# Performance work log

Measured on AMD Instinct MI355X. Metric: run time of the kernel, lower is better.

## Reference

```python
import jax, jax.numpy as jnp
import numpy as np

N_NODES = 100000
N_EDGES = 3200000
N_GRAPHS = 256
IN_CH = 8
HID = 64


def _gcn_conv(x, W, b, src, dst, n):
    # PyG GCNConv default: add self-loops, symmetric normalization.
    # out_i = sum_{j->i} d_i^-1/2 d_j^-1/2 (xW)_j + (1/d_i)(xW)_i + b
    xw = x @ W                                     # [N, out]
    deg = jax.ops.segment_sum(jnp.ones_like(dst, dtype=xw.dtype), dst,
                              num_segments=n) + 1.0  # +1 for self-loop
    dinv = jax.lax.rsqrt(deg)
    norm = dinv[src] * dinv[dst]                   # [E]
    agg = jax.ops.segment_sum(xw[src] * norm[:, None], dst, num_segments=n)
    agg = agg + xw * (1.0 / deg)[:, None]          # self-loop term (norm = 1/deg)
    return agg + b


def setup_inputs() -> dict:
    key = jax.random.key(0)
    ks = jax.random.split(key, 12)
    x = jax.random.normal(ks[0], (N_NODES, IN_CH), dtype=jnp.float32)
    edge_index = jax.random.randint(ks[1], (2, N_EDGES), 0, N_NODES, dtype=jnp.int64)
    batch = jnp.sort(jax.random.randint(ks[2], (N_NODES,), 0, N_GRAPHS, dtype=jnp.int64))

    def glorot(k, fan_in, fan_out):
        s = jnp.sqrt(2.0 / (fan_in + fan_out)).astype(jnp.float32)
        return jax.random.normal(k, (fan_in, fan_out), dtype=jnp.float32) * s

    return {
        "x": x, "edge_index": edge_index, "batch": batch,
        "W1": glorot(ks[3], IN_CH, HID), "b1": jnp.zeros((HID,), jnp.float32),
        "W2": glorot(ks[4], HID, 2 * HID), "b2": jnp.zeros((2 * HID,), jnp.float32),
        "W3": glorot(ks[5], 2 * HID, HID), "b3": jnp.zeros((HID,), jnp.float32),
        "Wl1": glorot(ks[6], HID, HID // 2), "bl1": jnp.zeros((HID // 2,), jnp.float32),
        "Wl2": glorot(ks[7], HID // 2, 1), "bl2": jnp.zeros((1,), jnp.float32),
    }


def reference(x, edge_index, batch, W1, b1, W2, b2, W3, b3, Wl1, bl1, Wl2, bl2):
    src, dst = edge_index[0], edge_index[1]
    h = jax.nn.relu(_gcn_conv(x, W1, b1, src, dst, N_NODES))
    h = jax.nn.relu(_gcn_conv(h, W2, b2, src, dst, N_NODES))
    h = jax.nn.relu(_gcn_conv(h, W3, b3, src, dst, N_NODES))
    # global mean pool over graphs
    sums = jax.ops.segment_sum(h, batch, num_segments=N_GRAPHS)
    cnts = jax.ops.segment_sum(jnp.ones((N_NODES,), h.dtype), batch, num_segments=N_GRAPHS)
    g = sums / jnp.maximum(cnts, 1.0)[:, None]     # [G, HID]
    g = jax.nn.relu(g @ Wl1 + bl1)
    out = g @ Wl2 + bl2                            # [G, 1]
    return out[:, 0]
```

## Files before the change

### kernel.cpp

```cpp
#include <hip/hip_runtime.h>
#include <hip/hip_bf16.h>

#define N_NODES 100000
#define N_EDGES 3200000
#define N_GRAPHS 256
#define NB_BUCKETS 196
#define BSHIFT 9
#define NBLK 256
#define SCAN_BLKS 49
#define CSR_CAP 22528

#define OFF_SUMS      0u
#define OFF_CNTF      65536u
#define ZERO_BYTES    66560u
#define OFF_HIST      66560u
#define OFF_BSUM      267264u
#define OFF_ROWPTR    267776u
#define OFF_DINV      668160u
#define OFF_COL       1068544u
#define OFF_XS1       13868544u
#define OFF_BUFQ      20268544u
#define OFF_BUFR      45868544u
#define OFF_BUFP      71468544u
#define OFF_PAIRS     OFF_BUFP

typedef __attribute__((ext_vector_type(8))) short bf16x8;
typedef __attribute__((ext_vector_type(4))) float f32x4;

__device__ __forceinline__ unsigned short f2bf(float f) {
    unsigned u = __float_as_uint(f);
    return (unsigned short)((u + 0x7fffu + ((u >> 16) & 1u)) >> 16);
}

__device__ __forceinline__ float bf2f(unsigned short h) {
    return __uint_as_float(((unsigned)h) << 16);
}

__device__ __forceinline__ void acc_bf8(uint4 v, float m, float* a) {
    a[0] += m * __uint_as_float(v.x << 16);
    a[1] += m * __uint_as_float(v.x & 0xffff0000u);
    a[2] += m * __uint_as_float(v.y << 16);
    a[3] += m * __uint_as_float(v.y & 0xffff0000u);
    a[4] += m * __uint_as_float(v.z << 16);
    a[5] += m * __uint_as_float(v.z & 0xffff0000u);
    a[6] += m * __uint_as_float(v.w << 16);
    a[7] += m * __uint_as_float(v.w & 0xffff0000u);
}

__global__ __launch_bounds__(256) void hist_kernel(const int* __restrict__ dst,
                                                   int* __restrict__ hist,
                                                   int* __restrict__ zbase,
                                                   int E, int epb) {
    __shared__ int h[NB_BUCKETS];
    int t = threadIdx.x, blk = blockIdx.x;
    int gid = blk * 256 + t;
    if (gid < (int)(ZERO_BYTES / 4)) zbase[gid] = 0;
    if (t < NB_BUCKETS) h[t] = 0;
    __syncthreads();
    int e0 = blk * epb, e1 = min(e0 + epb, E);
    for (int e = e0 + t; e < e1; e += 256)
        atomicAdd(&h[__builtin_nontemporal_load(&dst[e]) >> BSHIFT], 1);
    __syncthreads();
    if (t < NB_BUCKETS) hist[t * NBLK + blk] = h[t];
}

__global__ __launch_bounds__(1024) void scanhA_kernel(int* __restrict__ hist,
                                                      int* __restrict__ bsum) {
    __shared__ int s[1024];
    int t = threadIdx.x;
    int i = blockIdx.x * 1024 + t;
    int v = hist[i];
    s[t] = v;
    __syncthreads();
    for (int off = 1; off < 1024; off <<= 1) {
        int add = (t >= off) ? s[t - off] : 0;
        __syncthreads();
        s[t] += add;
        __syncthreads();
    }
    hist[i] = s[t] - v;
    if (t == 1023) bsum[blockIdx.x] = s[t];
}

__global__ __launch_bounds__(256) void bin_kernel(const int* __restrict__ src,
                                                  const int* __restrict__ dst,
                                                  const int* __restrict__ hist,
                                                  const int* __restrict__ bsum,
                                                  int* __restrict__ packed, int E, int epb) {
    __shared__ int cur[NB_BUCKETS];
    __shared__ int boffL[SCAN_BLKS];
    int t = threadIdx.x, blk = blockIdx.x;
    if (t < 64) {
        int orig = (t < SCAN_BLKS) ? bsum[t] : 0;
        int v = orig;
        for (int off = 1; off < 64; off <<= 1) {
            int up = __shfl_up(v, off);
            if (t >= off) v += up;
        }
        if (t < SCAN_BLKS) boffL[t] = v - orig;
    }
    __syncthreads();
    if (t < NB_BUCKETS) {
        int i = t * NBLK + blk;
        cur[t] = hist[i] + boffL[i >> 10];
    }
    __syncthreads();
    int e0 = blk * epb, e1 = min(e0 + epb, E);
    for (int e = e0 + t; e < e1; e += 256) {
        int d = __builtin_nontemporal_load(&dst[e]);
        int sv = __builtin_nontemporal_load(&src[e]);
        int pos = atomicAdd(&cur[d >> BSHIFT], 1);
        packed[pos] = ((d & 511) << 17) | sv;
    }
}

__global__ __launch_bounds__(512) void csr_kernel(const int* __restrict__ packed,
                                                  const int* __restrict__ hist,
                                                  const int* __restrict__ bsum,
                                                  const float* __restrict__ x,
                                                  int* __restrict__ row_ptr,
                                                  float* __restrict__ dinv,
                                                  unsigned short* __restrict__ xs1,
                                                  int* __restrict__ col, int E) {
    __shared__ int cntL[512];
    __shared__ int rsL[512];
    __shared__ int fillL[512];
    __shared__ int boffL[SCAN_BLKS];
    __shared__ int srcL[CSR_CAP];
    int t = threadIdx.x, b = blockIdx.x;
    int lo = b << BSHIFT;
    int nloc = min(512, N_NODES - lo);
    cntL[t] = 0;
    fillL[t] = 0;
    if (t < 64) {
        int orig = (t < SCAN_BLKS) ? bsum[t] : 0;
        int v = orig;
        for (int off = 1; off < 64; off <<= 1) {
            int up = __shfl_up(v, off);
            if (t >= off) v += up;
        }
        if (t < SCAN_BLKS) boffL[t] = v - orig;
    }
    __syncthreads();
    int i0 = b * NBLK;
    int start = hist[i0] + boffL[i0 >> 10];
    int end;
    if (b == NB_BUCKETS - 1) end = E;
    else {
        int i1 = (b + 1) * NBLK;
        end = hist[i1] + boffL[i1 >> 10];
    }
    for (int e = start + t; e < end; e += 512)
        atomicAdd(&cntL[packed[e] >> 17], 1);
    __syncthreads();
    int v = cntL[t];
    __syncthreads();
    for (int off = 1; off < 512; off <<= 1) {
        int add = (t >= off) ? cntL[t - off] : 0;
        __syncthreads();
        cntL[t] += add;
        __syncthreads();
    }
    int rowstart = start + cntL[t] - v;
    rsL[t] = rowstart;
    if (t < nloc) {
        int node = lo + t;
        row_ptr[node] = rowstart;
        float d = rsqrtf((float)(v + 1));
        dinv[node] = d;
        const float4* xv = reinterpret_cast<const float4*>(x) + node * 2;
        float4 xa = xv[0], xb = xv[1];
        uint4 p;
        p.x = (unsigned)f2bf(xa.x * d) | ((unsigned)f2bf(xa.y * d) << 16);
        p.y = (unsigned)f2bf(xa.z * d) | ((unsigned)f2bf(xa.w * d) << 16);
        p.z = (unsigned)f2bf(xb.x * d) | ((unsigned)f2bf(xb.y * d) << 16);
        p.w = (unsigned)f2bf(xb.z * d) | ((unsigned)f2bf(xb.w * d) << 16);
        *reinterpret_cast<uint4*>(&xs1[node * 8]) = p;
    }
    if (b == NB_BUCKETS - 1 && t == 0) row_ptr[N_NODES] = E;
    __syncthreads();
    for (int e = start + t; e < end; e += 512) {
        int p = packed[e];
        int dl = p >> 17;
        int pos = rsL[dl] + atomicAdd(&fillL[dl], 1);
        int rel = pos - start;
        if (rel < CSR_CAP) srcL[rel] = p & 0x1FFFF;
        else col[pos] = p & 0x1FFFF;
    }
    __syncthreads();
    int lim = min(end - start, CSR_CAP);
    for (int i = t; i < lim; i += 512)
        col[start + i] = srcL[i];
}

__global__ __launch_bounds__(256) void agg8g1_kernel(
        const unsigned short* __restrict__ xs, const int* __restrict__ row_ptr,
        const int* __restrict__ col, const float* __restrict__ dinv,
        const float* __restrict__ W1, const float* __restrict__ b1,
        unsigned short* __restrict__ xs2, int n) {
    int wave = threadIdx.x >> 6;
    int node = blockIdx.x * 4 + wave;
    if (node >= n) return;
    int lane = threadIdx.x & 63;
    int f = lane & 7;
    int s = lane >> 3;
    float w[8];
    float bias = b1[lane];
#pragma unroll
    for (int k = 0; k < 8; ++k) w[k] = W1[k * 64 + lane];
    int e0 = row_ptr[node], e1 = row_ptr[node + 1];
    float a = (s == 0) ? bf2f(xs[node * 8 + f]) : 0.0f;
    int base = e0;
    for (; e1 - base > 48; base += 48) {
#pragma unroll
        for (int g = 0; g < 6; ++g) {
            int c = __builtin_nontemporal_load(&col[base + 8 * g + s]);
            a += bf2f(xs[c * 8 + f]);
        }
    }
    int rem = e1 - base;
    if (rem > 0) {
        int e1m1 = e1 - 1;
        bool g4 = rem > 32, g5 = rem > 40;
        int i0 = base + s,      i1 = base + 8 + s,  i2 = base + 16 + s;
        int i3 = base + 24 + s, i4 = base + 32 + s, i5 = base + 40 + s;
        int c0 = __builtin_nontemporal_load(&col[min(i0, e1m1)]);
        int c1 = __builtin_nontemporal_load(&col[min(i1, e1m1)]);
        int c2 = __builtin_nontemporal_load(&col[min(i2, e1m1)]);
        int c3 = __builtin_nontemporal_load(&col[min(i3, e1m1)]);
        int c4 = 0, c5 = 0;
        if (g4) c4 = __builtin_nontemporal_load(&col[min(i4, e1m1)]);
        if (g5) c5 = __builtin_nontemporal_load(&col[min(i5, e1m1)]);
        float v0 = bf2f(xs[c0 * 8 + f]);
        float v1 = bf2f(xs[c1 * 8 + f]);
        float v2 = bf2f(xs[c2 * 8 + f]);
        float v3 = bf2f(xs[c3 * 8 + f]);
        float v4 = 0.f, v5 = 0.f;
        if (g4) v4 = bf2f(xs[c4 * 8 + f]);
        if (g5) v5 = bf2f(xs[c5 * 8 + f]);
        a += ((i0 < e1) ? v0 : 0.f) + ((i1 < e1) ? v1 : 0.f);
        a += ((i2 < e1) ? v2 : 0.f) + ((i3 < e1) ? v3 : 0.f);
        if (g4) a += (i4 < e1) ? v4 : 0.f;
        if (g5) a += (i5 < e1) ? v5 : 0.f;
    }
    a += __shfl_xor(a, 8);
    a += __shfl_xor(a, 16);
    a += __shfl_xor(a, 32);
    float d = dinv[node];
    float zd = a * d;
    float acc = bias;
#pragma unroll
    for (int k = 0; k < 8; ++k) acc += __shfl(zd, k) * w[k];
    xs2[node * 64 + lane] = f2bf(d * fmaxf(acc, 0.0f));
}

__global__ __launch_bounds__(256) void agg64bf_kernel(
        const unsigned short* __restrict__ xs, const int* __restrict__ row_ptr,
        const int* __restrict__ col, const float* __restrict__ dinv,
        unsigned short* __restrict__ z, int n0, int n1) {
    int wave = threadIdx.x >> 6;
    int node = n0 + blockIdx.x * 4 + wave;
    if (node >= n1) return;
    int lane = threadIdx.x & 63;
    int j = lane >> 3, l = lane & 7;
    int e0 = row_ptr[node], e1 = row_ptr[node + 1];
    float a[8] = {0.f, 0.f, 0.f, 0.f, 0.f, 0.f, 0.f, 0.f};
    uint4 sv = *reinterpret_cast<const uint4*>(&xs[node * 64 + 8 * l]);
    int base = e0;
    for (; e1 - base > 48; base += 32) {
        int s0 = __builtin_nontemporal_load(&col[base + j]);
        int s1 = __builtin_nontemporal_load(&col[base + 8 + j]);
        int s2 = __builtin_nontemporal_load(&col[base + 16 + j]);
        int s3 = __builtin_nontemporal_load(&col[base + 24 + j]);
        uint4 v0 = *reinterpret_cast<const uint4*>(&xs[s0 * 64 + 8 * l]);
        uint4 v1 = *reinterpret_cast<const uint4*>(&xs[s1 * 64 + 8 * l]);
        uint4 v2 = *reinterpret_cast<const uint4*>(&xs[s2 * 64 + 8 * l]);
        uint4 v3 = *reinterpret_cast<const uint4*>(&xs[s3 * 64 + 8 * l]);
        acc_bf8(v0, 1.f, a); acc_bf8(v1, 1.f, a);
        acc_bf8(v2, 1.f, a); acc_bf8(v3, 1.f, a);
    }
    int rem = e1 - base;
    if (rem > 0) {
        int e1m1 = e1 - 1;
        bool g4 = rem > 32, g5 = rem > 40;
        int i0 = base + j,      i1 = base + 8 + j;
        int i2 = base + 16 + j, i3 = base + 24 + j;
        int i4 = base + 32 + j, i5 = base + 40 + j;
        int c0 = __builtin_nontemporal_load(&col[min(i0, e1m1)]);
        int c1 = __builtin_nontemporal_load(&col[min(i1, e1m1)]);
        int c2 = __builtin_nontemporal_load(&col[min(i2, e1m1)]);
        int c3 = __builtin_nontemporal_load(&col[min(i3, e1m1)]);
        int c4 = 0, c5 = 0;
        if (g4) c4 = __builtin_nontemporal_load(&col[min(i4, e1m1)]);
        if (g5) c5 = __builtin_nontemporal_load(&col[min(i5, e1m1)]);
        uint4 v0 = *reinterpret_cast<const uint4*>(&xs[c0 * 64 + 8 * l]);
        uint4 v1 = *reinterpret_cast<const uint4*>(&xs[c1 * 64 + 8 * l]);
        uint4 v2 = *reinterpret_cast<const uint4*>(&xs[c2 * 64 + 8 * l]);
        uint4 v3 = *reinterpret_cast<const uint4*>(&xs[c3 * 64 + 8 * l]);
        uint4 v4, v5;
        if (g4) v4 = *reinterpret_cast<const uint4*>(&xs[c4 * 64 + 8 * l]);
        if (g5) v5 = *reinterpret_cast<const uint4*>(&xs[c5 * 64 + 8 * l]);
        acc_bf8(v0, (i0 < e1) ? 1.f : 0.f, a);
        acc_bf8(v1, (i1 < e1) ? 1.f : 0.f, a);
        acc_bf8(v2, (i2 < e1) ? 1.f : 0.f, a);
        acc_bf8(v3, (i3 < e1) ? 1.f : 0.f, a);
        if (g4) acc_bf8(v4, (i4 < e1) ? 1.f : 0.f, a);
        if (g5) acc_bf8(v5, (i5 < e1) ? 1.f : 0.f, a);
    }
    acc_bf8(sv, (j == 0) ? 1.f : 0.f, a);
#pragma unroll
    for (int k = 0; k < 8; ++k) {
        a[k] += __shfl_xor(a[k], 8);
        a[k] += __shfl_xor(a[k], 16);
        a[k] += __shfl_xor(a[k], 32);
    }
    if (j == 0) {
        float d = dinv[node];
        uint4 p;
        p.x = (unsigned)f2bf(a[0] * d) | ((unsigned)f2bf(a[1] * d) << 16);
        p.y = (unsigned)f2bf(a[2] * d) | ((unsigned)f2bf(a[3] * d) << 16);
        p.z = (unsigned)f2bf(a[4] * d) | ((unsigned)f2bf(a[5] * d) << 16);
        p.w = (unsigned)f2bf(a[6] * d) | ((unsigned)f2bf(a[7] * d) << 16);
        *reinterpret_cast<uint4*>(&z[node * 64 + 8 * l]) = p;
    }
}

template <int K, int M, bool BIAS, bool RELU, bool SCALE, bool BF16OUT>
__global__ __launch_bounds__(256) void mgemm_kernel(
        const unsigned short* __restrict__ X, const float* __restrict__ W,
        const float* __restrict__ b, const float* __restrict__ dinv,
        float* __restrict__ Y, int nrows) {
    constexpr int KP = K + 8;
    constexpr int NT = M / 16;
    constexpr int KS = K / 32;
    __shared__ unsigned short Wt[M * KP];
    int tid = threadIdx.x;
    for (int i = tid; i < K * M; i += 256) {
        int k = i / M, m = i % M;
        Wt[m * KP + k] = f2bf(W[i]);
    }
    __syncthreads();
    int wave = tid >> 6, lane = tid & 63;
    int row0 = blockIdx.x * 64 + wave * 16;
    int hl = lane >> 4, ll = lane & 15;
    int arow = min(row0 + ll, nrows - 1);
    bf16x8 afrag[KS];
#pragma unroll
    for (int ks = 0; ks < KS; ++ks)
        afrag[ks] = *reinterpret_cast<const bf16x8*>(&X[arow * K + ks * 32 + hl * 8]);
    f32x4 acc[NT];
#pragma unroll
    for (int nt = 0; nt < NT; ++nt) {
        float bv = BIAS ? b[nt * 16 + ll] : 0.0f;
        acc[nt] = {bv, bv, bv, bv};
    }
#pragma unroll
    for (int nt = 0; nt < NT; ++nt) {
#pragma unroll
        for (int ks = 0; ks < KS; ++ks) {
            bf16x8 bfrag = *reinterpret_cast<const bf16x8*>(
                &Wt[(nt * 16 + ll) * KP + ks * 32 + hl * 8]);
            acc[nt] = __builtin_amdgcn_mfma_f32_16x16x32_bf16(
                afrag[ks], bfrag, acc[nt], 0, 0, 0);
        }
    }
#pragma unroll
    for (int r = 0; r < 4; ++r) {
        int row = row0 + hl * 4 + r;
        if (row < nrows) {
            float d = SCALE ? dinv[row] : 1.0f;
#pragma unroll
            for (int nt = 0; nt < NT; ++nt) {
                float v = acc[nt][r];
                if constexpr (RELU) v = fmaxf(v, 0.0f);
                if constexpr (SCALE) v *= d;
                if constexpr (BF16OUT)
                    reinterpret_cast<unsigned short*>(Y)[row * M + nt * 16 + ll] = f2bf(v);
                else
                    Y[row * M + nt * 16 + ll] = v;
            }
        }
    }
}

#define POOL_NPB 128
__global__ __launch_bounds__(256) void pool_kernel(
        const unsigned short* __restrict__ z3, const float* __restrict__ b3,
        const int* __restrict__ batch, float* __restrict__ sums,
        float* __restrict__ cntf, int n) {
    int wave = threadIdx.x >> 6;
    int lane = threadIdx.x & 63;
    int node0 = blockIdx.x * POOL_NPB + wave * 32;
    int nodeEnd = min(node0 + 32, n);
    if (node0 >= n) return;
    float bias = b3[lane];
    float acc = 0.0f, cnt = 0.0f;
    int curg = -1;
    for (int node = node0; node < nodeEnd; ++node) {
        int g = batch[node];
        if (g != curg) {
            if (curg >= 0) {
                atomicAdd(&sums[curg * 64 + lane], acc);
                if (lane == 0) atomicAdd(&cntf[curg], cnt);
            }
            curg = g; acc = 0.0f; cnt = 0.0f;
        }
        acc += fmaxf(bf2f(z3[node * 64 + lane]) + bias, 0.0f);
        cnt += 1.0f;
    }
    if (curg >= 0) {
        atomicAdd(&sums[curg * 64 + lane], acc);
        if (lane == 0) atomicAdd(&cntf[curg], cnt);
    }
}

__global__ void mlp_kernel(const float* __restrict__ sums, const float* __restrict__ cntf,
                           const float* __restrict__ Wl1, const float* __restrict__ bl1,
                           const float* __restrict__ Wl2, const float* __restrict__ bl2,
                           float* __restrict__ out) {
    __shared__ float gv[64];
    __shared__ float hid[32];
    int g = blockIdx.x, t = threadIdx.x;
    float denom = fmaxf(cntf[g], 1.0f);
    gv[t] = sums[g * 64 + t] / denom;
    __syncthreads();
    if (t < 32) {
        float a = bl1[t];
#pragma unroll
        for (int k = 0; k < 64; ++k) a += gv[k] * Wl1[k * 32 + t];
        hid[t] = fmaxf(a, 0.0f);
    }
    __syncthreads();
    if (t == 0) {
        float o = bl2[0];
#pragma unroll
        for (int k = 0; k < 32; ++k) o += hid[k] * Wl2[k];
        out[g] = o;
    }
}

extern "C" void kernel_launch(void* const* d_in, const int* in_sizes, int n_in,
                              void* d_out, int out_size, void* d_ws, size_t ws_size,
                              hipStream_t stream) {
    const float* x   = (const float*)d_in[0];
    const int* ei    = (const int*)d_in[1];
    const int* batch = (const int*)d_in[2];
    const float* W1  = (const float*)d_in[3];
    const float* b1  = (const float*)d_in[4];
    const float* W2  = (const float*)d_in[5];
    const float* b2  = (const float*)d_in[6];
    const float* W3  = (const float*)d_in[7];
    const float* b3  = (const float*)d_in[8];
    const float* Wl1 = (const float*)d_in[9];
    const float* bl1 = (const float*)d_in[10];
    const float* Wl2 = (const float*)d_in[11];
    const float* bl2 = (const float*)d_in[12];
    float* out = (float*)d_out;

    const int N = N_NODES;
    const int E = in_sizes[1] / 2;
    const int* src = ei;
    const int* dst = ei + E;

    char* ws = (char*)d_ws;
    float* sums    = (float*)(ws + OFF_SUMS);
    float* cntf    = (float*)(ws + OFF_CNTF);
    int*   hist    = (int*)(ws + OFF_HIST);
    int*   bsum    = (int*)(ws + OFF_BSUM);
    int*   row_ptr = (int*)(ws + OFF_ROWPTR);
    float* dinv    = (float*)(ws + OFF_DINV);
    int*   col     = (int*)(ws + OFF_COL);
    unsigned short* xs1 = (unsigned short*)(ws + OFF_XS1);
    float* bufQ    = (float*)(ws + OFF_BUFQ);
    float* bufR    = (float*)(ws + OFF_BUFR);
    float* bufP    = (float*)(ws + OFF_BUFP);
    int*   packed  = (int*)(ws + OFF_PAIRS);

    int epb = (E + NBLK - 1) / NBLK;
    hist_kernel<<<NBLK, 256, 0, stream>>>(dst, hist, (int*)ws, E, epb);
    scanhA_kernel<<<SCAN_BLKS, 1024, 0, stream>>>(hist, bsum);
    bin_kernel<<<NBLK, 256, 0, stream>>>(src, dst, hist, bsum, packed, E, epb);
    csr_kernel<<<NB_BUCKETS, 512, 0, stream>>>(packed, hist, bsum, x,
                                               row_ptr, dinv, xs1, col, E);

    agg8g1_kernel<<<(N + 3) / 4, 256, 0, stream>>>(xs1, row_ptr, col, dinv, W1, b1,
                                                   (unsigned short*)bufQ, N);

    agg64bf_kernel<<<(N + 3) / 4, 256, 0, stream>>>(
        (const unsigned short*)bufQ, row_ptr, col, dinv,
        (unsigned short*)bufR, 0, N);
    mgemm_kernel<64, 128, true, true, false, true><<<1563, 256, 0, stream>>>(
        (const unsigned short*)bufR, W2, b2, nullptr, bufP, N);

    mgemm_kernel<128, 64, false, false, true, true><<<1563, 256, 0, stream>>>(
        (const unsigned short*)bufP, W3, nullptr, dinv, bufR, N);
    agg64bf_kernel<<<(N + 3) / 4, 256, 0, stream>>>(
        (const unsigned short*)bufR, row_ptr, col, dinv,
        (unsigned short*)bufQ, 0, N);

    pool_kernel<<<(N + POOL_NPB - 1) / POOL_NPB, 256, 0, stream>>>(
        (const unsigned short*)bufQ, b3, batch, sums, cntf, N);
    mlp_kernel<<<N_GRAPHS, 64, 0, stream>>>(sums, cntf, Wl1, bl1, Wl2, bl2, out);
}
```

Baseline: 355.7 us.

## Fuse layer-2/3 GEMMs via LDS and fold mean-pool into final aggregation

Merges the two dense transforms into one kernel that keeps the intermediate 128-wide activations in shared memory, removing a global write and read of that buffer and one launch. Folds bias, ReLU and graph pooling into the last neighbor-aggregation kernel, dropping the separate pool kernel and its read of the layer output. The fused pooling issues one atomic per node per feature instead of batching runs of nodes per graph, raising atomic traffic and contention. The larger LDS footprint in the GEMM kernel may lower occupancy.

New measurement: 664.2 us. +86.7%, slower.

```diff
diff --git a/kernel.cpp b/kernel.cpp
--- a/kernel.cpp
+++ b/kernel.cpp
@@ -254,15 +254,20 @@
     xs2[node * 64 + lane] = f2bf(d * fmaxf(acc, 0.0f));
 }
 
+template <bool POOL>
 __global__ __launch_bounds__(256) void agg64bf_kernel(
         const unsigned short* __restrict__ xs, const int* __restrict__ row_ptr,
         const int* __restrict__ col, const float* __restrict__ dinv,
-        unsigned short* __restrict__ z, int n0, int n1) {
+        unsigned short* __restrict__ z, const float* __restrict__ b3,
+        const int* __restrict__ batch, float* __restrict__ sums,
+        float* __restrict__ cntf, int n) {
     int wave = threadIdx.x >> 6;
-    int node = n0 + blockIdx.x * 4 + wave;
-    if (node >= n1) return;
+    int node = blockIdx.x * 4 + wave;
+    if (node >= n) return;
     int lane = threadIdx.x & 63;
     int j = lane >> 3, l = lane & 7;
+    float b3v = 0.0f;
+    if constexpr (POOL) b3v = b3[8 * l + j];
     int e0 = row_ptr[node], e1 = row_ptr[node + 1];
     float a[8] = {0.f, 0.f, 0.f, 0.f, 0.f, 0.f, 0.f, 0.f};
     uint4 sv = *reinterpret_cast<const uint4*>(&xs[node * 64 + 8 * l]);
@@ -314,103 +319,104 @@
         a[k] += __shfl_xor(a[k], 16);
         a[k] += __shfl_xor(a[k], 32);
     }
-    if (j == 0) {
-        float d = dinv[node];
-        uint4 p;
-        p.x = (unsigned)f2bf(a[0] * d) | ((unsigned)f2bf(a[1] * d) << 16);
-        p.y = (unsigned)f2bf(a[2] * d) | ((unsigned)f2bf(a[3] * d) << 16);
-        p.z = (unsigned)f2bf(a[4] * d) | ((unsigned)f2bf(a[5] * d) << 16);
-        p.w = (unsigned)f2bf(a[6] * d) | ((unsigned)f2bf(a[7] * d) << 16);
-        *reinterpret_cast<uint4*>(&z[node * 64 + 8 * l]) = p;
-    }
-}
-
-template <int K, int M, bool BIAS, bool RELU, bool SCALE, bool BF16OUT>
-__global__ __launch_bounds__(256) void mgemm_kernel(
-        const unsigned short* __restrict__ X, const float* __restrict__ W,
-        const float* __restrict__ b, const float* __restrict__ dinv,
-        float* __restrict__ Y, int nrows) {
-    constexpr int KP = K + 8;
-    constexpr int NT = M / 16;
-    constexpr int KS = K / 32;
-    __shared__ unsigned short Wt[M * KP];
+    float d = dinv[node];
+    if constexpr (POOL) {
+        float s01 = (j & 1) ? a[1] : a[0];
+        float s23 = (j & 1) ? a[3] : a[2];
+        float s45 = (j & 1) ? a[5] : a[4];
+        float s67 = (j & 1) ? a[7] : a[6];
+        float s03 = (j & 2) ? s23 : s01;
+        float s47 = (j & 2) ? s67 : s45;
+        float av  = (j & 4) ? s47 : s03;
+        int g = batch[node];
+        float h3 = fmaxf(av * d + b3v, 0.0f);
+        atomicAdd(&sums[g * 64 + 8 * l + j], h3);
+        if (lane == 0) atomicAdd(&cntf[g], 1.0f);
+    } else {
+        if (j == 0) {
+            uint4 p;
+            p.x = (unsigned)f2bf(a[0] * d) | ((unsigned)f2bf(a[1] * d) << 16);
+            p.y = (unsigned)f2bf(a[2] * d) | ((unsigned)f2bf(a[3] * d) << 16);
+            p.z = (unsigned)f2bf(a[4] * d) | ((unsigned)f2bf(a[5] * d) << 16);
+            p.w = (unsigned)f2bf(a[6] * d) | ((unsigned)f2bf(a[7] * d) << 16);
+            *reinterpret_cast<uint4*>(&z[node * 64 + 8 * l]) = p;
+        }
+    }
+}
+
+__global__ __launch_bounds__(256) void mgemm23_kernel(
+        const unsigned short* __restrict__ X,
+        const float* __restrict__ W2, const float* __restrict__ b2,
+        const float* __restrict__ W3, const float* __restrict__ dinv,
+        unsigned short* __restrict__ Y,
+        int nrows) {
+    __shared__ unsigned short Wt2[128 * 72];
+    __shared__ unsigned short Wt3[64 * 136];
+    __shared__ unsigned short h2L[64 * 136];
     int tid = threadIdx.x;
-    for (int i = tid; i < K * M; i += 256) {
-        int k = i / M, m = i % M;
-        Wt[m * KP + k] = f2bf(W[i]);
+    for (int i = tid; i < 64 * 128; i += 256) {
+        int k = i / 128, m = i % 128;
+        Wt2[m * 72 + k] = f2bf(W2[i]);
+    }
+    for (int i = tid; i < 128 * 64; i += 256) {
+        int k = i / 64, m = i % 64;
+        Wt3[m * 136 + k] = f2bf(W3[i]);
     }
     __syncthreads();
     int wave = tid >> 6, lane = tid & 63;
     int row0 = blockIdx.x * 64 + wave * 16;
     int hl = lane >> 4, ll = lane & 15;
     int arow = min(row0 + ll, nrows - 1);
-    bf16x8 afrag[KS];
-#pragma unroll
-    for (int ks = 0; ks < KS; ++ks)
-        afrag[ks] = *reinterpret_cast<const bf16x8*>(&X[arow * K + ks * 32 + hl * 8]);
-    f32x4 acc[NT];
-#pragma unroll
-    for (int nt = 0; nt < NT; ++nt) {
-        float bv = BIAS ? b[nt * 16 + ll] : 0.0f;
-        acc[nt] = {bv, bv, bv, bv};
-    }
-#pragma unroll
-    for (int nt = 0; nt < NT; ++nt) {
-#pragma unroll
-        for (int ks = 0; ks < KS; ++ks) {
-            bf16x8 bfrag = *reinterpret_cast<const bf16x8*>(
-                &Wt[(nt * 16 + ll) * KP + ks * 32 + hl * 8]);
-            acc[nt] = __builtin_amdgcn_mfma_f32_16x16x32_bf16(
-                afrag[ks], bfrag, acc[nt], 0, 0, 0);
+    bf16x8 af0 = *reinterpret_cast<const bf16x8*>(&X[arow * 64 + hl * 8]);
+    bf16x8 af1 = *reinterpret_cast<const bf16x8*>(&X[arow * 64 + 32 + hl * 8]);
+    f32x4 acc1[8];
+#pragma unroll
+    for (int nt = 0; nt < 8; ++nt) {
+        float bv = b2[nt * 16 + ll];
+        acc1[nt] = {bv, bv, bv, bv};
+    }
+#pragma unroll
+    for (int nt = 0; nt < 8; ++nt) {
+        bf16x8 b0 = *reinterpret_cast<const bf16x8*>(&Wt2[(nt * 16 + ll) * 72 + hl * 8]);
+        bf16x8 b1 = *reinterpret_cast<const bf16x8*>(&Wt2[(nt * 16 + ll) * 72 + 32 + hl * 8]);
+        acc1[nt] = __builtin_amdgcn_mfma_f32_16x16x32_bf16(af0, b0, acc1[nt], 0, 0, 0);
+        acc1[nt] = __builtin_amdgcn_mfma_f32_16x16x32_bf16(af1, b1, acc1[nt], 0, 0, 0);
+    }
+#pragma unroll
+    for (int nt = 0; nt < 8; ++nt) {
+#pragma unroll
+        for (int r = 0; r < 4; ++r) {
+            float v = fmaxf(acc1[nt][r], 0.0f);
+            h2L[(wave * 16 + hl * 4 + r) * 136 + nt * 16 + ll] = f2bf(v);
+        }
+    }
+    __syncthreads();
+    bf16x8 af2[4];
+#pragma unroll
+    for (int ks = 0; ks < 4; ++ks)
+        af2[ks] = *reinterpret_cast<const bf16x8*>(
+            &h2L[(wave * 16 + ll) * 136 + ks * 32 + hl * 8]);
+    f32x4 acc2[4];
+#pragma unroll
+    for (int nt = 0; nt < 4; ++nt) acc2[nt] = {0.f, 0.f, 0.f, 0.f};
+#pragma unroll
+    for (int nt = 0; nt < 4; ++nt) {
+#pragma unroll
+        for (int ks = 0; ks < 4; ++ks) {
+            bf16x8 bf = *reinterpret_cast<const bf16x8*>(
+                &Wt3[(nt * 16 + ll) * 136 + ks * 32 + hl * 8]);
+            acc2[nt] = __builtin_amdgcn_mfma_f32_16x16x32_bf16(af2[ks], bf, acc2[nt], 0, 0, 0);
         }
     }
 #pragma unroll
     for (int r = 0; r < 4; ++r) {
         int row = row0 + hl * 4 + r;
         if (row < nrows) {
-            float d = SCALE ? dinv[row] : 1.0f;
-#pragma unroll
-            for (int nt = 0; nt < NT; ++nt) {
-                float v = acc[nt][r];
-                if constexpr (RELU) v = fmaxf(v, 0.0f);
-                if constexpr (SCALE) v *= d;
-                if constexpr (BF16OUT)
-                    reinterpret_cast<unsigned short*>(Y)[row * M + nt * 16 + ll] = f2bf(v);
-                else
-                    Y[row * M + nt * 16 + ll] = v;
-            }
-        }
-    }
-}
-
-#define POOL_NPB 128
-__global__ __launch_bounds__(256) void pool_kernel(
-        const unsigned short* __restrict__ z3, const float* __restrict__ b3,
-        const int* __restrict__ batch, float* __restrict__ sums,
-        float* __restrict__ cntf, int n) {
-    int wave = threadIdx.x >> 6;
-    int lane = threadIdx.x & 63;
-    int node0 = blockIdx.x * POOL_NPB + wave * 32;
-    int nodeEnd = min(node0 + 32, n);
-    if (node0 >= n) return;
-    float bias = b3[lane];
-    float acc = 0.0f, cnt = 0.0f;
-    int curg = -1;
-    for (int node = node0; node < nodeEnd; ++node) {
-        int g = batch[node];
-        if (g != curg) {
-            if (curg >= 0) {
-                atomicAdd(&sums[curg * 64 + lane], acc);
-                if (lane == 0) atomicAdd(&cntf[curg], cnt);
-            }
-            curg = g; acc = 0.0f; cnt = 0.0f;
-        }
-        acc += fmaxf(bf2f(z3[node * 64 + lane]) + bias, 0.0f);
-        cnt += 1.0f;
-    }
-    if (curg >= 0) {
-        atomicAdd(&sums[curg * 64 + lane], acc);
-        if (lane == 0) atomicAdd(&cntf[curg], cnt);
+            float d = dinv[row];
+#pragma unroll
+            for (int nt = 0; nt < 4; ++nt)
+                Y[row * 64 + nt * 16 + ll] = f2bf(acc2[nt][r] * d);
+        }
     }
 }
 
@@ -471,9 +477,8 @@
     float* dinv    = (float*)(ws + OFF_DINV);
     int*   col     = (int*)(ws + OFF_COL);
     unsigned short* xs1 = (unsigned short*)(ws + OFF_XS1);
-    float* bufQ    = (float*)(ws + OFF_BUFQ);
-    float* bufR    = (float*)(ws + OFF_BUFR);
-    float* bufP    = (float*)(ws + OFF_BUFP);
+    unsigned short* bufQ = (unsigned short*)(ws + OFF_BUFQ);
+    unsigned short* bufR = (unsigned short*)(ws + OFF_BUFR);
     int*   packed  = (int*)(ws + OFF_PAIRS);
 
     int epb = (E + NBLK - 1) / NBLK;
@@ -484,21 +489,15 @@
                                                row_ptr, dinv, xs1, col, E);
 
     agg8g1_kernel<<<(N + 3) / 4, 256, 0, stream>>>(xs1, row_ptr, col, dinv, W1, b1,
-                                                   (unsigned short*)bufQ, N);
-
-    agg64bf_kernel<<<(N + 3) / 4, 256, 0, stream>>>(
-        (const unsigned short*)bufQ, row_ptr, col, dinv,
-        (unsigned short*)bufR, 0, N);
-    mgemm_kernel<64, 128, true, true, false, true><<<1563, 256, 0, stream>>>(
-        (const unsigned short*)bufR, W2, b2, nullptr, bufP, N);
-
-    mgemm_kernel<128, 64, false, false, true, true><<<1563, 256, 0, stream>>>(
-        (const unsigned short*)bufP, W3, nullptr, dinv, bufR, N);
-    agg64bf_kernel<<<(N + 3) / 4, 256, 0, stream>>>(
-        (const unsigned short*)bufR, row_ptr, col, dinv,
-        (unsigned short*)bufQ, 0, N);
-
-    pool_kernel<<<(N + POOL_NPB - 1) / POOL_NPB, 256, 0, stream>>>(
-        (const unsigned short*)bufQ, b3, batch, sums, cntf, N);
+                                                   bufQ, N);
+
+    agg64bf_kernel<false><<<(N + 3) / 4, 256, 0, stream>>>(
+        bufQ, row_ptr, col, dinv, bufR, nullptr, nullptr, nullptr, nullptr, N);
+
+    mgemm23_kernel<<<1563, 256, 0, stream>>>(bufR, W2, b2, W3, dinv, bufQ, N);
+
+    agg64bf_kernel<true><<<(N + 3) / 4, 256, 0, stream>>>(
+        bufQ, row_ptr, col, dinv, nullptr, b3, batch, sums, cntf, N);
+
     mlp_kernel<<<N_GRAPHS, 64, 0, stream>>>(sums, cntf, Wl1, bl1, Wl2, bl2, out);
 }
```
